# Optimization experiments

Measured on AMD Instinct MI355X. Metric: run time of the kernel, lower is better.

Reference implementation:

```python
import jax, jax.numpy as jnp
import numpy as np

HIDDEN = 4096
LATENT = 32768


def setup_inputs() -> dict:
    key = jax.random.key(0)
    k1, k2, k3, k4, k5 = jax.random.split(key, 5)
    x = jax.random.normal(k1, (2, 2048, HIDDEN), dtype=jnp.float32)
    # learned params (loaded from checkpoint in the original; random here)
    pre_bias = jax.random.normal(k2, (HIDDEN,), dtype=jnp.float32) * 0.02
    latent_bias = jax.random.normal(k3, (LATENT,), dtype=jnp.float32) * 0.02
    # nn.Linear weights: encoder.weight [latent, hidden], decoder.weight [hidden, latent]
    enc_w = jax.random.normal(k4, (LATENT, HIDDEN), dtype=jnp.float32) / np.sqrt(HIDDEN)
    dec_w = jax.random.normal(k5, (HIDDEN, LATENT), dtype=jnp.float32) / np.sqrt(LATENT)
    return {"x": x, "pre_bias": pre_bias, "latent_bias": latent_bias,
            "enc_w": enc_w, "dec_w": dec_w, "k": 64}


def reference(x, pre_bias, latent_bias, enc_w, dec_w, k):
    B, S, H = x.shape
    L = enc_w.shape[0]
    # pre_acts = encoder(x - pre_bias) + latent_bias
    pre_acts = jnp.einsum('bsh,lh->bsl', x - pre_bias, enc_w) + latent_bias
    # TopK sparsification: keep top-k values per token, zero elsewhere
    flat = pre_acts.reshape(B * S, L)
    vals, idx = jax.lax.top_k(flat, k)                       # [N,k]
    rows = jnp.arange(B * S)[:, None]                        # [N,1]
    latents = jnp.zeros_like(flat).at[rows, idx].set(vals).reshape(B, S, L)
    # x_hat = decoder(latents) + pre_bias
    x_hat = jnp.einsum('bsl,hl->bsh', latents, dec_w) + pre_bias
    return latents, x_hat
```

## Files before the change

### kernel.cpp

```cpp
#include <hip/hip_runtime.h>
#include <hip/hip_fp16.h>

typedef unsigned short u16;
typedef unsigned int u32;
using f32x4 = __attribute__((ext_vector_type(4))) float;
using bf16x8 = __attribute__((ext_vector_type(8))) short;

#define M_TOK 4096
#define HID   4096
#define LAT   32768
#define TOPK  64

#define BM 256
#define BN 128
#define BK 32
#define NT (HID / BK)
#define LCAP 2048
#define CAND_T0 2.0f
#define WBAND 0.0625f

__device__ __forceinline__ u16 f2bf(float f) {
  u32 u = __builtin_bit_cast(u32, f);
  u32 r = 0x7fffu + ((u >> 16) & 1u);
  return (u16)((u + r) >> 16);
}

__global__ __launch_bounds__(256) void k_xs(const float* __restrict__ x,
                                            const float* __restrict__ pb,
                                            u16* __restrict__ xs) {
  size_t i = ((size_t)blockIdx.x * 256 + threadIdx.x) * 4;
  if (i >= (size_t)M_TOK * HID) return;
  float4 xv = *(const float4*)(x + i);
  float4 bv = *(const float4*)(pb + (i & (HID - 1)));
  ushort4 o;
  o.x = f2bf(xv.x - bv.x); o.y = f2bf(xv.y - bv.y);
  o.z = f2bf(xv.z - bv.z); o.w = f2bf(xv.w - bv.w);
  *(ushort4*)(xs + i) = o;
}

__global__ __launch_bounds__(256) void k_conv(const float* __restrict__ src,
                                              u16* __restrict__ dst, size_t n4) {
  size_t i = (size_t)blockIdx.x * 256 + threadIdx.x;
  size_t stride = (size_t)gridDim.x * 256;
  for (; i < n4; i += stride) {
    float4 v = ((const float4*)src)[i];
    ushort4 o;
    o.x = f2bf(v.x); o.y = f2bf(v.y); o.z = f2bf(v.z); o.w = f2bf(v.w);
    ((ushort4*)dst)[i] = o;
  }
}

__global__ __launch_bounds__(512, 4) void k_gemm(const u16* __restrict__ A,
                                                 const u16* __restrict__ B,
                                                 const float* __restrict__ lbias,
                                                 float2* __restrict__ lists,
                                                 int* __restrict__ cnt) {
  __shared__ __align__(16) u16 Asm[2][128][64];
  __shared__ __align__(16) u16 Bsm[2][64][64];
  const int tid = threadIdx.x;
  const int lane = tid & 63;
  const int wave = tid >> 6;
  const int wm = wave >> 1;
  const int wn = wave & 1;

  const int bid = blockIdx.x;
  const int wg = (bid & 7) * 512 + (bid >> 3);
  const int bm = (wg & 15) * BM;
  const int bn = (wg >> 4) * BN;

  const int sp = tid >> 3, sslot = tid & 7;
  const int ss0 = sslot ^ (sp & 7);
  const int sr = sp * 2 + (ss0 >> 2);
  const int sc = (ss0 & 3) << 3;
  const int sp2 = sp + 64;
  const int ss02 = sslot ^ (sp2 & 7);
  const int sr2 = sp2 * 2 + (ss02 >> 2);
  const int sc2 = (ss02 & 3) << 3;

  auto stage = [&](int t) {
    int b = t & 1;
    __builtin_amdgcn_global_load_lds(
        (const __attribute__((address_space(1))) void*)(
            A + (size_t)(bm + sr) * HID + t * BK + sc),
        (__attribute__((address_space(3))) void*)(&Asm[b][sp][sslot << 3]), 16, 0, 0);
    __builtin_amdgcn_global_load_lds(
        (const __attribute__((address_space(1))) void*)(
            A + (size_t)(bm + sr2) * HID + t * BK + sc2),
        (__attribute__((address_space(3))) void*)(&Asm[b][sp2][sslot << 3]), 16, 0, 0);
    if (sp < 64)
      __builtin_amdgcn_global_load_lds(
          (const __attribute__((address_space(1))) void*)(
              B + (size_t)(bn + sr) * HID + t * BK + sc),
          (__attribute__((address_space(3))) void*)(&Bsm[b][sp][sslot << 3]), 16, 0, 0);
    else
      __builtin_amdgcn_global_load_lds(
          (const __attribute__((address_space(1))) void*)(
              B + (size_t)(bn + sr - 128) * HID + t * BK + sc),
          (__attribute__((address_space(3))) void*)(&Bsm[b][sp - 64][sslot << 3]), 16, 0, 0);
  };

  const int chunk = lane >> 4;
  auto readA = [&](int b, int m) -> bf16x8 {
    int r = wm * 64 + m * 16 + (lane & 15);
    int p = r >> 1;
    int s = (((r & 1) << 2) + chunk) ^ (p & 7);
    return *(const bf16x8*)(&Asm[b][p][s << 3]);
  };
  auto readB = [&](int b, int n) -> bf16x8 {
    int r = wn * 64 + n * 16 + (lane & 15);
    int p = r >> 1;
    int s = (((r & 1) << 2) + chunk) ^ (p & 7);
    return *(const bf16x8*)(&Bsm[b][p][s << 3]);
  };

  f32x4 acc[4][4] = {};

  stage(0);
  __syncthreads();

#pragma unroll 1
  for (int t = 0; t < NT; ++t) {
    const int b = t & 1;
    if (t + 1 < NT) stage(t + 1);
    bf16x8 a[4], bb[4];
#pragma unroll
    for (int m = 0; m < 4; ++m) a[m] = readA(b, m);
#pragma unroll
    for (int n = 0; n < 4; ++n) bb[n] = readB(b, n);
#pragma unroll
    for (int m = 0; m < 4; ++m)
#pragma unroll
      for (int n = 0; n < 4; ++n)
        acc[m][n] = __builtin_amdgcn_mfma_f32_16x16x32_bf16(a[m], bb[n], acc[m][n], 0, 0, 0);
    __syncthreads();
  }

#pragma unroll
  for (int n = 0; n < 4; ++n) {
    int col = bn + wn * 64 + n * 16 + (lane & 15);
    float lb = lbias[col];
#pragma unroll
    for (int m = 0; m < 4; ++m) {
      int row = bm + wm * 64 + m * 16 + ((lane >> 4) << 2);
#pragma unroll
      for (int j = 0; j < 4; ++j) {
        float v = acc[m][n][j] + lb;
        if (v >= CAND_T0) {
          int p = atomicAdd(&cnt[row + j], 1);
          if (p < LCAP)
            lists[(size_t)(row + j) * LCAP + p] =
                make_float2(v, __builtin_bit_cast(float, col));
        }
      }
    }
  }
}

__global__ __launch_bounds__(256) void k_topk(
    const float2* __restrict__ lists, const int* __restrict__ cnt,
    const float* __restrict__ x,
    const float* __restrict__ pb,
    const float* __restrict__ enc_w,
    const float* __restrict__ lbias,
    int* __restrict__ oidx, float* __restrict__ oval) {
  const int row = blockIdx.x;
  const int tid = threadIdx.x;
  const int lane = tid & 63, wave = tid >> 6;

  __shared__ int cnum, innum, selnum;
  __shared__ float s_m;
  __shared__ int lidx[LCAP];
  __shared__ float laf[LCAP];
  __shared__ int cidx[352];
  __shared__ double cref[352];
  __shared__ int fidx[64];
  __shared__ float fval[64];

  const int n = min(cnt[row], LCAP);
  if (tid == 0) { s_m = -1e30f; cnum = 0; innum = 0; selnum = 0; }
  for (int j = tid; j < n; j += 256) {
    float2 e = lists[(size_t)row * LCAP + j];
    laf[j] = e.x;
    lidx[j] = __builtin_bit_cast(int, e.y);
  }
  __syncthreads();

  for (int j = tid; j < n; j += 256) {
    float aj = laf[j]; int ij = lidx[j];
    int rank = 0;
    for (int i2 = 0; i2 < n; ++i2) {
      float ai = laf[i2];
      rank += (ai > aj) || (ai == aj && lidx[i2] < ij);
    }
    if (rank == 63) s_m = aj;
  }
  __syncthreads();
  float mf = s_m;

  for (int j = tid; j < n; j += 256) {
    float aa = laf[j];
    if (aa > mf + WBAND) {
      int p = atomicAdd(&innum, 1);
      if (p < 64) { fidx[p] = lidx[j]; fval[p] = aa; }
    } else if (aa >= mf - WBAND) {
      int p = atomicAdd(&cnum, 1);
      if (p < 352) cidx[p] = lidx[j];
    }
  }
  __syncthreads();
  int nin = min(innum, 64);
  int nu = min(cnum, 352);

  const float* xrow = x + (size_t)row * HID;
  for (int cc = wave; cc < nu; cc += 4) {
    const float* wrow = enc_w + (size_t)cidx[cc] * HID;
    double s = 0.0;
    for (int i = lane * 4; i < HID; i += 256) {
      float4 wv = *(const float4*)(wrow + i);
      float4 xv = *(const float4*)(xrow + i);
      float4 bv = *(const float4*)(pb + i);
      s += ((double)xv.x - (double)bv.x) * (double)wv.x;
      s += ((double)xv.y - (double)bv.y) * (double)wv.y;
      s += ((double)xv.z - (double)bv.z) * (double)wv.z;
      s += ((double)xv.w - (double)bv.w) * (double)wv.w;
    }
#pragma unroll
    for (int off = 32; off > 0; off >>= 1) s += __shfl_down(s, off);
    if (lane == 0) cref[cc] = s + (double)lbias[cidx[cc]];
  }
  __syncthreads();

  int need = 64 - nin;
  for (int j = tid; j < nu; j += 256) {
    double rj = cref[j]; int ij = cidx[j];
    int rank = 0;
    for (int i2 = 0; i2 < nu; ++i2) {
      double ri = cref[i2];
      rank += (ri > rj) || (ri == rj && cidx[i2] < ij);
    }
    if (rank < need) {
      int p = atomicAdd(&selnum, 1);
      if (nin + p < 64) { fidx[nin + p] = ij; fval[nin + p] = (float)rj; }
    }
  }
  __syncthreads();

  if (tid < 64) {
    int my = fidx[tid]; float v = fval[tid];
    int rank = 0;
#pragma unroll
    for (int i2 = 0; i2 < 64; ++i2) rank += (fidx[i2] < my);
    oidx[row * 64 + rank] = my;
    oval[row * 64 + rank] = v;
  }
}

__global__ __launch_bounds__(256) void k_trans(const float* __restrict__ dw,
                                               u16* __restrict__ dt) {
  __shared__ float tile[64][65];
  int l0 = blockIdx.x * 64;
  int h0 = blockIdx.y * 64;
  int tx = threadIdx.x & 15;
  int ty = threadIdx.x >> 4;
#pragma unroll
  for (int i = 0; i < 4; ++i) {
    int r = ty + i * 16;
    float4 v = *(const float4*)(dw + (size_t)(h0 + r) * LAT + l0 + tx * 4);
    tile[r][tx * 4 + 0] = v.x; tile[r][tx * 4 + 1] = v.y;
    tile[r][tx * 4 + 2] = v.z; tile[r][tx * 4 + 3] = v.w;
  }
  __syncthreads();
#pragma unroll
  for (int i = 0; i < 4; ++i) {
    int r = ty + i * 16;
    ushort4 o;
    o.x = f2bf(tile[tx * 4 + 0][r]);
    o.y = f2bf(tile[tx * 4 + 1][r]);
    o.z = f2bf(tile[tx * 4 + 2][r]);
    o.w = f2bf(tile[tx * 4 + 3][r]);
    *(ushort4*)(dt + (size_t)(l0 + r) * HID + h0 + tx * 4) = o;
  }
}

__global__ __launch_bounds__(256) void k_decode(
    const int* __restrict__ oidx, const float* __restrict__ oval,
    const u16* __restrict__ dt, const float* __restrict__ pb,
    float* __restrict__ xh) {
  const int n = blockIdx.x, tid = threadIdx.x;
  __shared__ int sidx[64];
  __shared__ float sval[64];
  if (tid < 64) { sidx[tid] = oidx[n * 64 + tid]; sval[tid] = oval[n * 64 + tid]; }
  __syncthreads();
  const int h0 = tid * 16;
  float acc[16];
#pragma unroll
  for (int q = 0; q < 4; ++q) {
    float4 b = *(const float4*)(pb + h0 + q * 4);
    acc[q * 4 + 0] = b.x; acc[q * 4 + 1] = b.y;
    acc[q * 4 + 2] = b.z; acc[q * 4 + 3] = b.w;
  }
  for (int j = 0; j < 64; ++j) {
    float v = sval[j];
    const uint4* w = (const uint4*)(dt + (size_t)sidx[j] * HID + h0);
    uint4 p0 = w[0], p1 = w[1];
    u32 u[8] = {p0.x, p0.y, p0.z, p0.w, p1.x, p1.y, p1.z, p1.w};
#pragma unroll
    for (int q = 0; q < 8; ++q) {
      float lo = __builtin_bit_cast(float, u[q] << 16);
      float hi = __builtin_bit_cast(float, u[q] & 0xffff0000u);
      acc[q * 2 + 0] = fmaf(v, lo, acc[q * 2 + 0]);
      acc[q * 2 + 1] = fmaf(v, hi, acc[q * 2 + 1]);
    }
  }
#pragma unroll
  for (int q = 0; q < 4; ++q) {
    float4 o;
    o.x = acc[q * 4 + 0]; o.y = acc[q * 4 + 1];
    o.z = acc[q * 4 + 2]; o.w = acc[q * 4 + 3];
    *(float4*)(xh + (size_t)n * HID + h0 + q * 4) = o;
  }
}

__global__ __launch_bounds__(256) void k_lat(const int* __restrict__ oidx,
                                             const float* __restrict__ oval,
                                             float* __restrict__ lat) {
  const int n = blockIdx.x, tid = threadIdx.x;
  __shared__ int sidx[64];
  __shared__ float sval[64];
  if (tid < 64) { sidx[tid] = oidx[n * 64 + tid]; sval[tid] = oval[n * 64 + tid]; }
  float* row = lat + (size_t)n * LAT;
  float4 z = {0.f, 0.f, 0.f, 0.f};
  for (int q = tid; q < LAT / 4; q += 256) *(float4*)(row + q * 4) = z;
  __syncthreads();
  if (tid < 64) row[sidx[tid]] = sval[tid];
}

extern "C" void kernel_launch(void* const* d_in, const int* in_sizes, int n_in,
                              void* d_out, int out_size, void* d_ws, size_t ws_size,
                              hipStream_t stream) {
  const float* x = (const float*)d_in[0];
  const float* pre_bias = (const float*)d_in[1];
  const float* latent_bias = (const float*)d_in[2];
  const float* enc_w = (const float*)d_in[3];
  const float* dec_w = (const float*)d_in[4];

  float* latents = (float*)d_out;
  float* xhat = latents + (size_t)M_TOK * LAT;

  u16* xs = (u16*)xhat;
  u16* encb = (u16*)latents;
  float2* lists = (float2*)((char*)d_out + (size_t)M_TOK * LAT * 2);
  u16* decT = (u16*)latents;
  int* cnt = (int*)d_ws;
  int* oidx = (int*)((char*)d_ws + M_TOK * 4);
  float* oval = (float*)((char*)d_ws + M_TOK * 4 + (size_t)M_TOK * TOPK * 4);

  hipMemsetAsync(cnt, 0, M_TOK * 4, stream);
  k_xs<<<(M_TOK * HID / 4 + 255) / 256, 256, 0, stream>>>(x, pre_bias, xs);
  k_conv<<<4096, 256, 0, stream>>>(enc_w, encb, (size_t)LAT * HID / 4);
  k_gemm<<<(M_TOK / BM) * (LAT / BN), 512, 0, stream>>>(xs, encb, latent_bias, lists, cnt);
  k_topk<<<M_TOK, 256, 0, stream>>>(lists, cnt, x, pre_bias, enc_w, latent_bias, oidx, oval);
  k_trans<<<dim3(LAT / 64, HID / 64), 256, 0, stream>>>(dec_w, decT);
  k_decode<<<M_TOK, 256, 0, stream>>>(oidx, oval, decT, pre_bias, xhat);
  k_lat<<<M_TOK, 256, 0, stream>>>(oidx, oval, latents);
}
```

Before: 2.682 ms.

## Triple-buffer encoder GEMM with manual waitcnts and transpose tile shape

Swaps the encoder GEMM block tile from 256x128 to 128x256 and arranges the eight waves as 2x4. It moves from a double-buffered to a triple-buffered LDS pipeline, prefetching two K-steps ahead. Full __syncthreads barriers are replaced by explicit vmcnt/lgkmcnt waits, raw s_barrier, and s_setprio around the MFMA block, and LDS reads are issued through inline ds_read_b128. The aim is to hide global-to-LDS latency behind the MFMAs. In exchange, LDS use per block rises, which may lower occupancy, and the hand-written waitcnts make correctness depend on exact counts.

After: 2.487 ms. 1.08x faster.

```diff
diff --git a/kernel.cpp b/kernel.cpp
--- a/kernel.cpp
+++ b/kernel.cpp
@@ -5,14 +5,15 @@
 typedef unsigned int u32;
 using f32x4 = __attribute__((ext_vector_type(4))) float;
 using bf16x8 = __attribute__((ext_vector_type(8))) short;
+using u32x4 = __attribute__((ext_vector_type(4))) u32;
 
 #define M_TOK 4096
 #define HID   4096
 #define LAT   32768
 #define TOPK  64
 
-#define BM 256
-#define BN 128
+#define BM 128
+#define BN 256
 #define BK 32
 #define NT (HID / BK)
 #define LCAP 2048
@@ -55,18 +56,18 @@
                                                  const float* __restrict__ lbias,
                                                  float2* __restrict__ lists,
                                                  int* __restrict__ cnt) {
-  __shared__ __align__(16) u16 Asm[2][128][64];
-  __shared__ __align__(16) u16 Bsm[2][64][64];
+  __shared__ __align__(16) u16 Asm[3][64][64];
+  __shared__ __align__(16) u16 Bsm[3][128][64];
   const int tid = threadIdx.x;
   const int lane = tid & 63;
   const int wave = tid >> 6;
-  const int wm = wave >> 1;
-  const int wn = wave & 1;
+  const int wm = wave >> 2;
+  const int wn = wave & 3;
 
   const int bid = blockIdx.x;
   const int wg = (bid & 7) * 512 + (bid >> 3);
-  const int bm = (wg & 15) * BM;
-  const int bn = (wg >> 4) * BN;
+  const int bm = (wg & 31) * BM;
+  const int bn = (wg >> 5) * BN;
 
   const int sp = tid >> 3, sslot = tid & 7;
   const int ss0 = sslot ^ (sp & 7);
@@ -77,62 +78,72 @@
   const int sr2 = sp2 * 2 + (ss02 >> 2);
   const int sc2 = (ss02 & 3) << 3;
 
-  auto stage = [&](int t) {
-    int b = t & 1;
+  auto stage = [&](int t, int buf) {
     __builtin_amdgcn_global_load_lds(
         (const __attribute__((address_space(1))) void*)(
             A + (size_t)(bm + sr) * HID + t * BK + sc),
-        (__attribute__((address_space(3))) void*)(&Asm[b][sp][sslot << 3]), 16, 0, 0);
+        (__attribute__((address_space(3))) void*)(&Asm[buf][sp][sslot << 3]), 16, 0, 0);
     __builtin_amdgcn_global_load_lds(
         (const __attribute__((address_space(1))) void*)(
-            A + (size_t)(bm + sr2) * HID + t * BK + sc2),
-        (__attribute__((address_space(3))) void*)(&Asm[b][sp2][sslot << 3]), 16, 0, 0);
-    if (sp < 64)
-      __builtin_amdgcn_global_load_lds(
-          (const __attribute__((address_space(1))) void*)(
-              B + (size_t)(bn + sr) * HID + t * BK + sc),
-          (__attribute__((address_space(3))) void*)(&Bsm[b][sp][sslot << 3]), 16, 0, 0);
-    else
-      __builtin_amdgcn_global_load_lds(
-          (const __attribute__((address_space(1))) void*)(
-              B + (size_t)(bn + sr - 128) * HID + t * BK + sc),
-          (__attribute__((address_space(3))) void*)(&Bsm[b][sp - 64][sslot << 3]), 16, 0, 0);
+            B + (size_t)(bn + sr) * HID + t * BK + sc),
+        (__attribute__((address_space(3))) void*)(&Bsm[buf][sp][sslot << 3]), 16, 0, 0);
+    __builtin_amdgcn_global_load_lds(
+        (const __attribute__((address_space(1))) void*)(
+            B + (size_t)(bn + sr2) * HID + t * BK + sc2),
+        (__attribute__((address_space(3))) void*)(&Bsm[buf][sp2][sslot << 3]), 16, 0, 0);
   };
 
   const int chunk = lane >> 4;
-  auto readA = [&](int b, int m) -> bf16x8 {
+  auto readA = [&](int buf, int m) -> bf16x8 {
     int r = wm * 64 + m * 16 + (lane & 15);
     int p = r >> 1;
     int s = (((r & 1) << 2) + chunk) ^ (p & 7);
-    return *(const bf16x8*)(&Asm[b][p][s << 3]);
+    u32 off = (u32)(uintptr_t)(__attribute__((address_space(3))) const void*)(&Asm[buf][p][s << 3]);
+    u32x4 rv;
+    asm volatile("ds_read_b128 %0, %1" : "=v"(rv) : "v"(off));
+    return __builtin_bit_cast(bf16x8, rv);
   };
-  auto readB = [&](int b, int n) -> bf16x8 {
+  auto readB = [&](int buf, int n) -> bf16x8 {
     int r = wn * 64 + n * 16 + (lane & 15);
     int p = r >> 1;
     int s = (((r & 1) << 2) + chunk) ^ (p & 7);
-    return *(const bf16x8*)(&Bsm[b][p][s << 3]);
+    u32 off = (u32)(uintptr_t)(__attribute__((address_space(3))) const void*)(&Bsm[buf][p][s << 3]);
+    u32x4 rv;
+    asm volatile("ds_read_b128 %0, %1" : "=v"(rv) : "v"(off));
+    return __builtin_bit_cast(bf16x8, rv);
   };
 
   f32x4 acc[4][4] = {};
 
-  stage(0);
-  __syncthreads();
+#define BARRIER() asm volatile("s_barrier" ::: "memory")
+#define LGKM0() do { asm volatile("s_waitcnt lgkmcnt(0)"); \
+                     __builtin_amdgcn_sched_barrier(0); } while (0)
+#define VMCNT3() asm volatile("s_waitcnt vmcnt(3)" ::: "memory")
+#define VMCNT0() asm volatile("s_waitcnt vmcnt(0)" ::: "memory")
+
+  stage(0, 0); stage(1, 1);
+  VMCNT3();
+  BARRIER();
 
 #pragma unroll 1
   for (int t = 0; t < NT; ++t) {
-    const int b = t & 1;
-    if (t + 1 < NT) stage(t + 1);
+    const int buf = t - (t / 3) * 3;
+    if (t + 2 < NT) stage(t + 2, (t + 2) - ((t + 2) / 3) * 3);
     bf16x8 a[4], bb[4];
 #pragma unroll
-    for (int m = 0; m < 4; ++m) a[m] = readA(b, m);
-#pragma unroll
-    for (int n = 0; n < 4; ++n) bb[n] = readB(b, n);
+    for (int m = 0; m < 4; ++m) a[m] = readA(buf, m);
+#pragma unroll
+    for (int n = 0; n < 4; ++n) bb[n] = readB(buf, n);
+    LGKM0();
+    __builtin_amdgcn_s_setprio(1);
 #pragma unroll
     for (int m = 0; m < 4; ++m)
 #pragma unroll
       for (int n = 0; n < 4; ++n)
         acc[m][n] = __builtin_amdgcn_mfma_f32_16x16x32_bf16(a[m], bb[n], acc[m][n], 0, 0, 0);
-    __syncthreads();
+    __builtin_amdgcn_s_setprio(0);
+    if (t + 2 < NT) VMCNT3(); else VMCNT0();
+    BARRIER();
   }
 
 #pragma unroll
@@ -154,6 +165,10 @@
       }
     }
   }
+#undef BARRIER
+#undef LGKM0
+#undef VMCNT3
+#undef VMCNT0
 }
 
 __global__ __launch_bounds__(256) void k_topk(
```
